# Performance work log

Measured on AMD Instinct MI355X. Metric: run time of the kernel, lower is better.

The kernel has to match this reference:

```python
import jax, jax.numpy as jnp
import numpy as np

B, L, D, H = 2, 2048, 1024, 16
HD = D // H

def setup_inputs() -> dict:
    key = jax.random.key(0)
    ks = jax.random.split(key, 9)
    s = 1.0 / np.sqrt(D)
    return {
        "query": jax.random.normal(ks[0], (B, L, D), dtype=jnp.float32),
        "Wq": jax.random.uniform(ks[1], (D, D), jnp.float32, -s, s),
        "bq": jax.random.uniform(ks[2], (D,), jnp.float32, -s, s),
        "Wk": jax.random.uniform(ks[3], (D, D), jnp.float32, -s, s),
        "bk": jax.random.uniform(ks[4], (D,), jnp.float32, -s, s),
        "Wv": jax.random.uniform(ks[5], (D, D), jnp.float32, -s, s),
        "bv": jax.random.uniform(ks[6], (D,), jnp.float32, -s, s),
        "Wo": jax.random.uniform(ks[7], (D, D), jnp.float32, -s, s),
        "bo": jax.random.uniform(ks[8], (D,), jnp.float32, -s, s),
    }

def reference(query, Wq, bq, Wk, bk, Wv, bv, Wo, bo):
    # self-attention: key_value = query. Linear: x @ W.T + b (torch convention)
    scale = HD ** -0.5
    q = (query @ Wq.T + bq).reshape(B, L, H, HD).transpose(0, 2, 1, 3)  # (B,H,L,hd)
    k = (query @ Wk.T + bk).reshape(B, L, H, HD).transpose(0, 2, 1, 3)
    v = (query @ Wv.T + bv).reshape(B, L, H, HD).transpose(0, 2, 1, 3)
    logits = jnp.einsum('bhqd,bhkd->bhqk', q, k) * scale  # (B,H,Lq,Lk)
    attn = jax.nn.softmax(logits, axis=-1)
    out = jnp.einsum('bhqk,bhkd->bhqd', attn, v)
    out = out.transpose(0, 2, 1, 3).reshape(B, L, D)
    return out @ Wo.T + bo
```

## Files before the change

kernel.cpp:

```cpp
#include <hip/hip_runtime.h>

#define Bc 2
#define Lc 2048
#define Dc 1024
#define Hc 16
#define HDc 64
#define LOG2E 1.44269504088896340736f

typedef __bf16 bf16x8 __attribute__((ext_vector_type(8)));
typedef __bf16 bf16x2 __attribute__((ext_vector_type(2)));
typedef float f32x4 __attribute__((ext_vector_type(4)));
typedef unsigned short u16;
typedef unsigned int u32;
typedef unsigned long long u64;

__device__ __forceinline__ u16 f2bf(float x) {
    union { float f; u32 u; } c; c.f = x;
    u32 u = c.u + 0x7fffu + ((c.u >> 16) & 1u);
    return (u16)(u >> 16);
}

__device__ __forceinline__ u32 pkbf(float a, float b) {
#if __has_builtin(__builtin_amdgcn_cvt_pk_bf16_f32)
    union { bf16x2 v; u32 u; } c;
    c.v = __builtin_amdgcn_cvt_pk_bf16_f32(a, b);
    return c.u;
#else
    return (u32)f2bf(a) | ((u32)f2bf(b) << 16);
#endif
}

__device__ __forceinline__ float fexp2(float x) {
#if __has_builtin(__builtin_amdgcn_exp2f)
    return __builtin_amdgcn_exp2f(x);
#else
    return exp2f(x);
#endif
}

__device__ __forceinline__ void g2l16(const void* g, void* l) {
    __builtin_amdgcn_global_load_lds(
        (const __attribute__((address_space(1))) void*)g,
        (__attribute__((address_space(3))) void*)l, 16, 0, 0);
}

__global__ __launch_bounds__(256) void cast_bf16(
    const float* __restrict__ x,
    const float* __restrict__ wq, const float* __restrict__ wk,
    const float* __restrict__ wv, const float* __restrict__ wo,
    u16* __restrict__ xb, u16* __restrict__ wqb, u16* __restrict__ wkb,
    u16* __restrict__ wvb, u16* __restrict__ wob)
{
    const int i = blockIdx.x * 256 + threadIdx.x;
    const float* s; u16* d; int off;
    if (i < 1048576) { s = x; d = xb; off = i; }
    else {
        const int j = i - 1048576;
        const int sel = j >> 18;
        off = j & 262143;
        s = sel == 0 ? wq : sel == 1 ? wk : sel == 2 ? wv : wo;
        d = sel == 0 ? wqb : sel == 1 ? wkb : sel == 2 ? wvb : wob;
    }
    const float4 f = ((const float4*)s)[off];
    ushort4 o;
    o.x = f2bf(f.x); o.y = f2bf(f.y); o.z = f2bf(f.z); o.w = f2bf(f.w);
    ((ushort4*)d)[off] = o;
}

__device__ __forceinline__ void gemm_o_body(
    const u16* __restrict__ A, const u16* __restrict__ Bm,
    int row0, int col0, int K,
    f32x4 (&acc)[4][2], u16* As, u16* Bs)
{
    const int tid  = threadIdx.x;
    const int w    = tid >> 6;
    const int lane = tid & 63;
    const int l15  = lane & 15, quad = lane >> 4;
    const int srow = lane >> 3;
    const int sxor = ((lane & 7) ^ srow) << 3;
    const int wm   = (w & 1) << 6, wn = (w >> 1) << 5;
    const int l7   = l15 & 7;

    for (int k0 = 0; k0 < K; k0 += 64) {
        __syncthreads();
#pragma unroll
        for (int s = 0; s < 6; ++s) {
            const int c = w * 6 + s;
            if (c < 16) {
                const int rb = c * 8;
                g2l16(&A [(size_t)(row0 + rb + srow) * K + k0 + sxor], &As[rb * 64]);
            } else {
                const int rb = (c - 16) * 8;
                g2l16(&Bm[(size_t)(col0 + rb + srow) * K + k0 + sxor], &Bs[rb * 64]);
            }
        }
        __syncthreads();

#pragma unroll
        for (int kk = 0; kk < 2; ++kk) {
            bf16x8 af[4], bf[2];
#pragma unroll
            for (int i = 0; i < 4; ++i)
                af[i] = *(const bf16x8*)&As[(wm + i * 16 + l15) * 64 +
                                            (((kk * 4 + quad) ^ l7) << 3)];
#pragma unroll
            for (int j = 0; j < 2; ++j)
                bf[j] = *(const bf16x8*)&Bs[(wn + j * 16 + l15) * 64 +
                                            (((kk * 4 + quad) ^ l7) << 3)];
#pragma unroll
            for (int i = 0; i < 4; ++i)
#pragma unroll
                for (int j = 0; j < 2; ++j)
                    acc[i][j] = __builtin_amdgcn_mfma_f32_16x16x32_bf16(
                        af[i], bf[j], acc[i][j], 0, 0, 0);
        }
    }
}

__global__ __launch_bounds__(256) void gemm_qkv_bf16(
    const u16* __restrict__ Xb,
    const u16* __restrict__ Wqb, const u16* __restrict__ Wkb, const u16* __restrict__ Wvb,
    const float* __restrict__ bq, const float* __restrict__ bk, const float* __restrict__ bv,
    u16* __restrict__ qo, u16* __restrict__ ko, u16* __restrict__ vto)
{
    __shared__ __attribute__((aligned(16))) u16 As[128 * 64];
    __shared__ __attribute__((aligned(16))) u16 Bs[64 * 64];

    const int z = blockIdx.z;
    const int tid = threadIdx.x;
    const int w = tid >> 6, lane = tid & 63;
    const int l15 = lane & 15, quad = lane >> 4;
    const int wm = (w & 1) << 6, wn = (w >> 1) << 5;

    f32x4 acc[4][2];
#pragma unroll
    for (int i = 0; i < 4; ++i)
#pragma unroll
        for (int j = 0; j < 2; ++j)
#pragma unroll
            for (int r = 0; r < 4; ++r) acc[i][j][r] = 0.0f;

    if (z == 2) {
        const int row0 = (blockIdx.x & 31) << 7;
        const int col0 = ((blockIdx.y << 1) | (blockIdx.x >> 5)) << 6;
        gemm_o_body(Xb, Wvb, row0, col0, Dc, acc, As, Bs);

        const int b = row0 >> 11;
#pragma unroll
        for (int j = 0; j < 2; ++j) {
            const int n = col0 + wn + j * 16 + l15;
            const float bj = bv[n];
            const int hh = n >> 6, hd = n & 63;
            u16* vbase = vto + (((size_t)(b * Hc + hh) * HDc + hd) << 11);
#pragma unroll
            for (int i = 0; i < 4; ++i) {
                const int l = (row0 + wm + i * 16 + quad * 4) & (Lc - 1);
                uint2 pr;
                pr.x = pkbf(acc[i][j][0] + bj, acc[i][j][1] + bj);
                pr.y = pkbf(acc[i][j][2] + bj, acc[i][j][3] + bj);
                *(uint2*)&vbase[l] = pr;
            }
        }
        return;
    }

    const u16*   W    = z == 0 ? Wqb : Wkb;
    const float* bias = z == 0 ? bq  : bk;
    u16*         outp = z == 0 ? qo  : ko;
    const int row0 = blockIdx.y << 7;
    const int col0 = blockIdx.x << 6;
    gemm_o_body(W, Xb, row0, col0, Dc, acc, As, Bs);

    const float qs = z == 0 ? 0.125f * LOG2E : 1.0f;
    const int h = (row0 + wm) >> 6;
    float4 b4[4];
#pragma unroll
    for (int i = 0; i < 4; ++i)
        b4[i] = *(const float4*)&bias[row0 + wm + i * 16 + quad * 4];

#pragma unroll
    for (int j = 0; j < 2; ++j) {
        const int tok = col0 + wn + j * 16 + l15;
        const int bb = tok >> 11, ll = tok & (Lc - 1);
        u16* obase = outp + (((size_t)(bb * Hc + h) * Lc + ll) << 6);
#pragma unroll
        for (int i = 0; i < 4; ++i) {
            uint2 pr;
            pr.x = pkbf((acc[i][j][0] + b4[i].x) * qs, (acc[i][j][1] + b4[i].y) * qs);
            pr.y = pkbf((acc[i][j][2] + b4[i].z) * qs, (acc[i][j][3] + b4[i].w) * qs);
            *(uint2*)&obase[i * 16 + quad * 4] = pr;
        }
    }
}

__global__ __launch_bounds__(512) void attn_mfma(
    const u16* __restrict__ q, const u16* __restrict__ k,
    const u16* __restrict__ vt, u16* __restrict__ out)
{
    __shared__ __attribute__((aligned(16))) u16 smem[17408];
    u16* Ks0 = smem;
    u16* Vs0 = smem + 8192;

    const int tid = threadIdx.x;
    const int w = tid >> 6, lane = tid & 63;
    const int l15 = lane & 15, quad = lane >> 4;
    const int bh = blockIdx.x & 31;
    const int qt = blockIdx.x >> 5;
    const int h  = bh & (Hc - 1);
    const int b  = bh >> 4;
    const int l0 = qt << 7;
    const int wq = w & 3;
    const int hf = w >> 2;

    const size_t bhs = (size_t)(b * Hc + h) * (Lc * HDc);
    const u16* qb = q  + bhs;
    const u16* kb = k  + bhs;
    const u16* vb = vt + bhs;

    bf16x8 qf[2][2];
#pragma unroll
    for (int mt = 0; mt < 2; ++mt) {
        const size_t row = (size_t)(l0 + wq * 32 + mt * 16 + l15) * HDc;
        qf[mt][0] = *(const bf16x8*)&qb[row + quad * 8];
        qf[mt][1] = *(const bf16x8*)&qb[row + 32 + quad * 8];
    }

    const int srow  = lane >> 2;
    const int sunit = lane & 3;
    const int gd = (l15 >> 1) & 3;

    f32x4 oacc[2][4];
    float l_i[2] = {0.0f, 0.0f};
#pragma unroll
    for (int mt = 0; mt < 2; ++mt)
#pragma unroll
        for (int dt = 0; dt < 4; ++dt)
#pragma unroll
            for (int r = 0; r < 4; ++r) oacc[mt][dt][r] = 0.0f;

    for (int kt = 0; kt < Lc; kt += 128) {
        __syncthreads();
#pragma unroll
        for (int i = 0; i < 4; ++i) {
            const int c = w * 4 + i;
            if (c < 16) {
                const int p = c >> 3, g = c & 7;
                const int row = g * 16 + srow;
                g2l16(&kb[(size_t)(kt + row) * HDc + p * 32 +
                          ((sunit ^ ((row >> 1) & 3)) << 3)],
                      &Ks0[p * 4096 + g * 512]);
            } else {
                const int cc = c - 16;
                const int cp = cc >> 2, g = cc & 3;
                const int row = g * 16 + srow;
                g2l16(&vb[(size_t)row * Lc + kt + cp * 32 +
                          ((sunit ^ ((row >> 1) & 3)) << 3)],
                      &Vs0[cp * 2048 + g * 512]);
            }
        }
        __syncthreads();

        f32x4 st[2][4];
        __builtin_amdgcn_s_setprio(1);
#pragma unroll
        for (int t = 0; t < 4; ++t) {
            const int j   = (hf * 4 + t) * 16 + l15;
            const int off = j * 32 + ((quad ^ gd) << 3);
            const bf16x8 kf0 = *(const bf16x8*)&Ks0[off];
            const bf16x8 kf1 = *(const bf16x8*)&Ks0[4096 + off];
#pragma unroll
            for (int mt = 0; mt < 2; ++mt) {
                f32x4 z = {0.0f, 0.0f, 0.0f, 0.0f};
                z = __builtin_amdgcn_mfma_f32_16x16x32_bf16(kf0, qf[mt][0], z, 0, 0, 0);
                st[mt][t] = __builtin_amdgcn_mfma_f32_16x16x32_bf16(kf1, qf[mt][1], z, 0, 0, 0);
            }
        }
        __builtin_amdgcn_s_setprio(0);

        u32 pk[2][4][2];
#pragma unroll
        for (int mt = 0; mt < 2; ++mt) {
            f32x4 s4 = {0.0f, 0.0f, 0.0f, 0.0f};
#pragma unroll
            for (int t = 0; t < 4; ++t) {
                f32x4 p;
#pragma unroll
                for (int r = 0; r < 4; ++r) p[r] = fexp2(st[mt][t][r]);
                s4 += p;
                pk[mt][t][0] = pkbf(p[0], p[1]);
                pk[mt][t][1] = pkbf(p[2], p[3]);
            }
            l_i[mt] += s4[0] + s4[1] + s4[2] + s4[3];
        }

        __builtin_amdgcn_s_setprio(1);
#pragma unroll
        for (int cpl = 0; cpl < 2; ++cpl) {
            const int cp = hf * 2 + cpl;
            union { bf16x8 v; u32 uw[4]; } pf0, pf1;
            pf0.uw[0] = pk[0][2 * cpl][0];     pf0.uw[1] = pk[0][2 * cpl][1];
            pf0.uw[2] = pk[0][2 * cpl + 1][0]; pf0.uw[3] = pk[0][2 * cpl + 1][1];
            pf1.uw[0] = pk[1][2 * cpl][0];     pf1.uw[1] = pk[1][2 * cpl][1];
            pf1.uw[2] = pk[1][2 * cpl + 1][0]; pf1.uw[3] = pk[1][2 * cpl + 1][1];
#pragma unroll
            for (int dt = 0; dt < 4; ++dt) {
                const int base = cp * 2048 + (dt * 16 + l15) * 32 + ((quad & 1) << 2);
                union { bf16x8 v; u64 d[2]; } vf;
                vf.d[0] = *(const u64*)&Vs0[base + (((quad >> 1) ^ gd) << 3)];
                vf.d[1] = *(const u64*)&Vs0[base + (((2 + (quad >> 1)) ^ gd) << 3)];
                oacc[0][dt] = __builtin_amdgcn_mfma_f32_16x16x32_bf16(
                    vf.v, pf0.v, oacc[0][dt], 0, 0, 0);
                oacc[1][dt] = __builtin_amdgcn_mfma_f32_16x16x32_bf16(
                    vf.v, pf1.v, oacc[1][dt], 0, 0, 0);
            }
        }
        __builtin_amdgcn_s_setprio(0);
    }

    __syncthreads();
    float* co = (float*)smem;
    float* cl = (float*)(smem + 16384);
    if (w >= 4) {
        const int base = (w - 4) * 64 + lane;
#pragma unroll
        for (int mt = 0; mt < 2; ++mt)
#pragma unroll
            for (int dt = 0; dt < 4; ++dt)
#pragma unroll
                for (int r = 0; r < 4; ++r)
                    co[(mt * 16 + dt * 4 + r) * 256 + base] = oacc[mt][dt][r];
        cl[base]       = l_i[0];
        cl[256 + base] = l_i[1];
    }
    __syncthreads();
    if (w >= 4) return;
    {
        const int base = w * 64 + lane;
#pragma unroll
        for (int mt = 0; mt < 2; ++mt)
#pragma unroll
            for (int dt = 0; dt < 4; ++dt)
#pragma unroll
                for (int r = 0; r < 4; ++r)
                    oacc[mt][dt][r] += co[(mt * 16 + dt * 4 + r) * 256 + base];
        l_i[0] += cl[base];
        l_i[1] += cl[256 + base];
    }

#pragma unroll
    for (int mt = 0; mt < 2; ++mt) {
        float l = l_i[mt];
        l += __shfl_xor(l, 16);
        l += __shfl_xor(l, 32);
        const float inv = 1.0f / l;
        const int lrow = l0 + wq * 32 + mt * 16 + l15;
        u16* ob = out + ((size_t)(b * Lc + lrow)) * Dc + h * HDc;
#pragma unroll
        for (int dt = 0; dt < 4; ++dt) {
            uint2 pr;
            pr.x = pkbf(oacc[mt][dt][0] * inv, oacc[mt][dt][1] * inv);
            pr.y = pkbf(oacc[mt][dt][2] * inv, oacc[mt][dt][3] * inv);
            *(uint2*)&ob[dt * 16 + quad * 4] = pr;
        }
    }
}

__global__ __launch_bounds__(256) void gemm_o_bf16(
    const u16* __restrict__ Ab, const u16* __restrict__ Wob,
    const float* __restrict__ bo, float* __restrict__ out)
{
    __shared__ __attribute__((aligned(16))) u16 As[128 * 64];
    __shared__ __attribute__((aligned(16))) u16 Bs[64 * 64];
    const int row0 = blockIdx.y << 7;
    const int col0 = blockIdx.x << 6;

    f32x4 acc[4][2];
#pragma unroll
    for (int i = 0; i < 4; ++i)
#pragma unroll
        for (int j = 0; j < 2; ++j)
#pragma unroll
            for (int r = 0; r < 4; ++r) acc[i][j][r] = 0.0f;

    gemm_o_body(Wob, Ab, row0, col0, Dc, acc, As, Bs);

    const int tid = threadIdx.x;
    const int w = tid >> 6, lane = tid & 63;
    const int l15 = lane & 15, quad = lane >> 4;
    const int wm = (w & 1) << 6, wn = (w >> 1) << 5;

    float4 b4[4];
#pragma unroll
    for (int i = 0; i < 4; ++i)
        b4[i] = *(const float4*)&bo[row0 + wm + i * 16 + quad * 4];

#pragma unroll
    for (int j = 0; j < 2; ++j) {
        const int tok = col0 + wn + j * 16 + l15;
        float* obase = out + (size_t)tok * Dc + row0 + wm;
#pragma unroll
        for (int i = 0; i < 4; ++i) {
            float4 o;
            o.x = acc[i][j][0] + b4[i].x; o.y = acc[i][j][1] + b4[i].y;
            o.z = acc[i][j][2] + b4[i].z; o.w = acc[i][j][3] + b4[i].w;
            *(float4*)&obase[i * 16 + quad * 4] = o;
        }
    }
}

extern "C" void kernel_launch(void* const* d_in, const int* in_sizes, int n_in,
                              void* d_out, int out_size, void* d_ws, size_t ws_size,
                              hipStream_t stream)
{
    const float* query = (const float*)d_in[0];
    const float* Wq = (const float*)d_in[1];
    const float* bq = (const float*)d_in[2];
    const float* Wk = (const float*)d_in[3];
    const float* bk = (const float*)d_in[4];
    const float* Wv = (const float*)d_in[5];
    const float* bv = (const float*)d_in[6];
    const float* Wo = (const float*)d_in[7];
    const float* bo = (const float*)d_in[8];

    u16* ws = (u16*)d_ws;
    const size_t nX = (size_t)Bc * Lc * Dc;
    const size_t nW = (size_t)Dc * Dc;
    u16* xb  = ws;
    u16* wqb = xb + nX;
    u16* wkb = wqb + nW;
    u16* wvb = wkb + nW;
    u16* wob = wvb + nW;
    u16* q_w = wob + nW;
    u16* k_w = q_w + nX;
    u16* vt_w = k_w + nX;
    u16* a_w = vt_w + nX;

    cast_bf16<<<dim3(8192), 256, 0, stream>>>(query, Wq, Wk, Wv, Wo,
                                              xb, wqb, wkb, wvb, wob);
    gemm_qkv_bf16<<<dim3(64, 8, 3), 256, 0, stream>>>(xb, wqb, wkb, wvb,
                                                      bq, bk, bv, q_w, k_w, vt_w);
    attn_mfma<<<dim3(512), 512, 0, stream>>>(q_w, k_w, vt_w, a_w);
    gemm_o_bf16<<<dim3(64, 8), 256, 0, stream>>>(a_w, wob, bo, (float*)d_out);
}
```

Baseline: 194.5 us.

## Fuse Q and K projections into one block sharing the X tile

Q and K projections now run in the same workgroup. It loads the X tile once and computes both outputs with two accumulator sets, and the grid drops from three z-slices to two. This removes a redundant global load of X for K and halves the Q/K block count. In exchange, each block uses more registers (twice the accumulators) and more LDS (an extra A tile), which with launch_bounds(256,4) may cause spills or lower occupancy. The Q/K blocks also now do twice the work of the V blocks, so the grid becomes imbalanced.

```diff
diff --git a/kernel.cpp b/kernel.cpp
--- a/kernel.cpp
+++ b/kernel.cpp
@@ -117,13 +117,73 @@
     }
 }
 
-__global__ __launch_bounds__(256) void gemm_qkv_bf16(
+__device__ __forceinline__ void gemm_qk_body(
+    const u16* __restrict__ Aq, const u16* __restrict__ Ak,
+    const u16* __restrict__ Bm,
+    int row0, int col0, int K,
+    f32x4 (&accq)[4][2], f32x4 (&acck)[4][2],
+    u16* As1, u16* As2, u16* Bs)
+{
+    const int tid  = threadIdx.x;
+    const int w    = tid >> 6;
+    const int lane = tid & 63;
+    const int l15  = lane & 15, quad = lane >> 4;
+    const int srow = lane >> 3;
+    const int sxor = ((lane & 7) ^ srow) << 3;
+    const int wm   = (w & 1) << 6, wn = (w >> 1) << 5;
+    const int l7   = l15 & 7;
+
+    for (int k0 = 0; k0 < K; k0 += 64) {
+        __syncthreads();
+#pragma unroll
+        for (int s = 0; s < 10; ++s) {
+            const int c = w * 10 + s;
+            if (c < 16) {
+                const int rb = c * 8;
+                g2l16(&Aq[(size_t)(row0 + rb + srow) * K + k0 + sxor], &As1[rb * 64]);
+            } else if (c < 32) {
+                const int rb = (c - 16) * 8;
+                g2l16(&Ak[(size_t)(row0 + rb + srow) * K + k0 + sxor], &As2[rb * 64]);
+            } else {
+                const int rb = (c - 32) * 8;
+                g2l16(&Bm[(size_t)(col0 + rb + srow) * K + k0 + sxor], &Bs[rb * 64]);
+            }
+        }
+        __syncthreads();
+
+#pragma unroll
+        for (int kk = 0; kk < 2; ++kk) {
+            bf16x8 afq[4], afk[4], bf[2];
+            const int ko = ((kk * 4 + quad) ^ l7) << 3;
+#pragma unroll
+            for (int i = 0; i < 4; ++i) {
+                afq[i] = *(const bf16x8*)&As1[(wm + i * 16 + l15) * 64 + ko];
+                afk[i] = *(const bf16x8*)&As2[(wm + i * 16 + l15) * 64 + ko];
+            }
+#pragma unroll
+            for (int j = 0; j < 2; ++j)
+                bf[j] = *(const bf16x8*)&Bs[(wn + j * 16 + l15) * 64 + ko];
+#pragma unroll
+            for (int i = 0; i < 4; ++i)
+#pragma unroll
+                for (int j = 0; j < 2; ++j) {
+                    accq[i][j] = __builtin_amdgcn_mfma_f32_16x16x32_bf16(
+                        afq[i], bf[j], accq[i][j], 0, 0, 0);
+                    acck[i][j] = __builtin_amdgcn_mfma_f32_16x16x32_bf16(
+                        afk[i], bf[j], acck[i][j], 0, 0, 0);
+                }
+        }
+    }
+}
+
+__global__ __launch_bounds__(256, 4) void gemm_qkv_bf16(
     const u16* __restrict__ Xb,
     const u16* __restrict__ Wqb, const u16* __restrict__ Wkb, const u16* __restrict__ Wvb,
     const float* __restrict__ bq, const float* __restrict__ bk, const float* __restrict__ bv,
     u16* __restrict__ qo, u16* __restrict__ ko, u16* __restrict__ vto)
 {
-    __shared__ __attribute__((aligned(16))) u16 As[128 * 64];
+    __shared__ __attribute__((aligned(16))) u16 As1[128 * 64];
+    __shared__ __attribute__((aligned(16))) u16 As2[128 * 64];
     __shared__ __attribute__((aligned(16))) u16 Bs[64 * 64];
 
     const int z = blockIdx.z;
@@ -132,18 +192,18 @@
     const int l15 = lane & 15, quad = lane >> 4;
     const int wm = (w & 1) << 6, wn = (w >> 1) << 5;
 
-    f32x4 acc[4][2];
-#pragma unroll
-    for (int i = 0; i < 4; ++i)
-#pragma unroll
-        for (int j = 0; j < 2; ++j)
-#pragma unroll
-            for (int r = 0; r < 4; ++r) acc[i][j][r] = 0.0f;
-
-    if (z == 2) {
+    if (z == 1) {
+        f32x4 acc[4][2];
+#pragma unroll
+        for (int i = 0; i < 4; ++i)
+#pragma unroll
+            for (int j = 0; j < 2; ++j)
+#pragma unroll
+                for (int r = 0; r < 4; ++r) acc[i][j][r] = 0.0f;
+
         const int row0 = (blockIdx.x & 31) << 7;
         const int col0 = ((blockIdx.y << 1) | (blockIdx.x >> 5)) << 6;
-        gemm_o_body(Xb, Wvb, row0, col0, Dc, acc, As, Bs);
+        gemm_o_body(Xb, Wvb, row0, col0, Dc, acc, As1, Bs);
 
         const int b = row0 >> 11;
 #pragma unroll
@@ -152,6 +212,8 @@
             const float bj = bv[n];
             const int hh = n >> 6, hd = n & 63;
             u16* vbase = vto + (((size_t)(b * Hc + hh) * HDc + hd) << 11);
+#pragma unroll
+            for (int i = 0; i < 2; ++i) { }
 #pragma unroll
             for (int i = 0; i < 4; ++i) {
                 const int l = (row0 + wm + i * 16 + quad * 4) & (Lc - 1);
@@ -164,31 +226,43 @@
         return;
     }
 
-    const u16*   W    = z == 0 ? Wqb : Wkb;
-    const float* bias = z == 0 ? bq  : bk;
-    u16*         outp = z == 0 ? qo  : ko;
+    f32x4 accq[4][2], acck[4][2];
+#pragma unroll
+    for (int i = 0; i < 4; ++i)
+#pragma unroll
+        for (int j = 0; j < 2; ++j)
+#pragma unroll
+            for (int r = 0; r < 4; ++r) { accq[i][j][r] = 0.0f; acck[i][j][r] = 0.0f; }
+
     const int row0 = blockIdx.y << 7;
     const int col0 = blockIdx.x << 6;
-    gemm_o_body(W, Xb, row0, col0, Dc, acc, As, Bs);
-
-    const float qs = z == 0 ? 0.125f * LOG2E : 1.0f;
+    gemm_qk_body(Wqb, Wkb, Xb, row0, col0, Dc, accq, acck, As1, As2, Bs);
+
+    const float qs = 0.125f * LOG2E;
     const int h = (row0 + wm) >> 6;
-    float4 b4[4];
-#pragma unroll
-    for (int i = 0; i < 4; ++i)
-        b4[i] = *(const float4*)&bias[row0 + wm + i * 16 + quad * 4];
+    float4 bq4[4], bk4[4];
+#pragma unroll
+    for (int i = 0; i < 4; ++i) {
+        bq4[i] = *(const float4*)&bq[row0 + wm + i * 16 + quad * 4];
+        bk4[i] = *(const float4*)&bk[row0 + wm + i * 16 + quad * 4];
+    }
 
 #pragma unroll
     for (int j = 0; j < 2; ++j) {
         const int tok = col0 + wn + j * 16 + l15;
         const int bb = tok >> 11, ll = tok & (Lc - 1);
-        u16* obase = outp + (((size_t)(bb * Hc + h) * Lc + ll) << 6);
+        const size_t obase = (((size_t)(bb * Hc + h) * Lc + ll) << 6);
+        u16* oq = qo + obase;
+        u16* ok = ko + obase;
 #pragma unroll
         for (int i = 0; i < 4; ++i) {
-            uint2 pr;
-            pr.x = pkbf((acc[i][j][0] + b4[i].x) * qs, (acc[i][j][1] + b4[i].y) * qs);
-            pr.y = pkbf((acc[i][j][2] + b4[i].z) * qs, (acc[i][j][3] + b4[i].w) * qs);
-            *(uint2*)&obase[i * 16 + quad * 4] = pr;
+            uint2 pq, pk2;
+            pq.x  = pkbf((accq[i][j][0] + bq4[i].x) * qs, (accq[i][j][1] + bq4[i].y) * qs);
+            pq.y  = pkbf((accq[i][j][2] + bq4[i].z) * qs, (accq[i][j][3] + bq4[i].w) * qs);
+            pk2.x = pkbf(acck[i][j][0] + bk4[i].x, acck[i][j][1] + bk4[i].y);
+            pk2.y = pkbf(acck[i][j][2] + bk4[i].z, acck[i][j][3] + bk4[i].w);
+            *(uint2*)&oq[i * 16 + quad * 4] = pq;
+            *(uint2*)&ok[i * 16 + quad * 4] = pk2;
         }
     }
 }
@@ -437,7 +511,7 @@
 
     cast_bf16<<<dim3(8192), 256, 0, stream>>>(query, Wq, Wk, Wv, Wo,
                                               xb, wqb, wkb, wvb, wob);
-    gemm_qkv_bf16<<<dim3(64, 8, 3), 256, 0, stream>>>(xb, wqb, wkb, wvb,
+    gemm_qkv_bf16<<<dim3(64, 8, 2), 256, 0, stream>>>(xb, wqb, wkb, wvb,
                                                       bq, bk, bv, q_w, k_w, vt_w);
     attn_mfma<<<dim3(512), 512, 0, stream>>>(q_w, k_w, vt_w, a_w);
     gemm_o_bf16<<<dim3(64, 8), 256, 0, stream>>>(a_w, wob, bo, (float*)d_out);
```

Measured after the change: 247.5 us. +27.2%, slower.
